# Optimization experiments

Measured on AMD Instinct MI355X. Metric: run time of the kernel, lower is better.

The kernel has to match this reference:

```python
import jax, jax.numpy as jnp
import numpy as np

N = 100000      # nodes
E = 3200000     # edges (avg degree 32)
IN_C = 256      # input feature dim
HID = 128       # hidden channels (= per-head dim, heads = 1)
L = 3           # num_layers_prop == num_layers_mlp
EPS = 1e-5


def _elu(x):
    return jnp.where(x > 0, x, jnp.expm1(x))


def _bn_eval(x, gamma, beta, mean, var):
    return (x - mean) * jax.lax.rsqrt(var + EPS) * gamma + beta


def _ln(x, gamma, beta):
    mu = jnp.mean(x, axis=-1, keepdims=True)
    var = jnp.var(x, axis=-1, keepdims=True)
    return (x - mu) * jax.lax.rsqrt(var + EPS) * gamma + beta


def setup_inputs() -> dict:
    key = jax.random.key(0)
    ks = jax.random.split(key, 12)
    s_in = np.float32(1.0 / np.sqrt(IN_C))
    s_h = np.float32(1.0 / np.sqrt(HID))
    return {
        "x": jax.random.normal(ks[0], (N, IN_C), jnp.float32),
        "edge_index": jax.random.randint(ks[1], (2, E), 0, N, jnp.int32),
        "mlp_W0": jax.random.normal(ks[2], (IN_C, HID), jnp.float32) * s_in,
        "mlp_b0": jnp.zeros((HID,), jnp.float32),
        "mlp_W": jax.random.normal(ks[3], (L - 1, HID, HID), jnp.float32) * s_h,
        "mlp_b": jnp.zeros((L - 1, HID), jnp.float32),
        "bn_gamma": jnp.ones((L, HID), jnp.float32),
        "bn_beta": jnp.zeros((L, HID), jnp.float32),
        "bn_mean": jnp.zeros((L, HID), jnp.float32),
        "bn_var": jnp.ones((L, HID), jnp.float32),
        "Wq": jax.random.normal(ks[4], (L, HID, HID), jnp.float32) * s_h,
        "bq": jnp.zeros((L, HID), jnp.float32),
        "Wk": jax.random.normal(ks[5], (L, HID, HID), jnp.float32) * s_h,
        "bk": jnp.zeros((L, HID), jnp.float32),
        "Wv": jax.random.normal(ks[6], (L, HID, HID), jnp.float32) * s_h,
        "bv": jnp.zeros((L, HID), jnp.float32),
        "Wg": jax.random.normal(ks[7], (L, HID, HID), jnp.float32) * s_h,
        "bg": jnp.zeros((L, HID), jnp.float32),
        "Wr": jax.random.normal(ks[8], (L, HID, HID), jnp.float32) * s_h,
        "br": jnp.zeros((L, HID), jnp.float32),
        "ln_gamma": jnp.ones((L, HID), jnp.float32),
        "ln_beta": jnp.zeros((L, HID), jnp.float32),
    }


def reference(x, edge_index, mlp_W0, mlp_b0, mlp_W, mlp_b, bn_gamma, bn_beta,
              bn_mean, bn_var, Wq, bq, Wk, bk, Wv, bv, Wg, bg, Wr, br,
              ln_gamma, ln_beta):
    n = x.shape[0]
    # --- mlp_in: Linear -> BN(eval) -> ELU, x3 (dropout p=0 skipped) ---
    h = _elu(_bn_eval(x @ mlp_W0 + mlp_b0, bn_gamma[0], bn_beta[0], bn_mean[0], bn_var[0]))
    for i in range(1, L):
        h = _elu(_bn_eval(h @ mlp_W[i - 1] + mlp_b[i - 1],
                          bn_gamma[i], bn_beta[i], bn_mean[i], bn_var[i]))

    # --- GCN edge normalization (shared across layers) ---
    row, col = edge_index[0], edge_index[1]
    deg = jax.ops.segment_sum(jnp.ones((E,), x.dtype), col, num_segments=n)
    val = jnp.sqrt(1.0 / deg[col]) * jnp.sqrt(1.0 / deg[row])
    val = jnp.nan_to_num(val, nan=0.0, posinf=0.0, neginf=0.0)

    # --- stacked TransConv layers (num_heads = 1) ---
    for i in range(L):
        prev = h
        q = h @ Wq[i] + bq[i]              # [N, M]
        k = h @ Wk[i] + bk[i]              # [N, M]
        v = h @ Wv[i] + bv[i]              # [N, D]
        qn = q / jnp.linalg.norm(q, axis=-1, keepdims=True)
        kn = k / jnp.linalg.norm(k, axis=-1, keepdims=True)
        kvs = kn.T @ v                     # [M, D]
        num = qn @ kvs + jnp.sum(v, axis=0)            # [N, D]
        denom = qn @ jnp.sum(kn, axis=0) + jnp.asarray(n, x.dtype)  # [N]
        attn_out = num / denom[:, None]    # heads=1 -> mean over heads is identity
        # sparse GCN: out[col] += val * gnn_in[row]
        g = h @ Wg[i] + bg[i]
        agg = jax.ops.segment_sum(val[:, None] * g[row], col, num_segments=n)
        out = attn_out + agg + (h @ Wr[i] + br[i])
        out = out + prev                   # outer residual in Transformer.forward
        h = _elu(_ln(out, ln_gamma[i], ln_beta[i]))
    return h
```

## Files before the change

### kernel.cpp

```cpp
#include <hip/hip_runtime.h>
#include <cstdint>
#include <cstddef>

#define HID 128
#define INC 256
#define NLAYER 3
#define SLOTS 96
#define P2G 16

static constexpr float EPS = 1e-5f;

typedef __attribute__((ext_vector_type(8))) short s16x8;
typedef __attribute__((ext_vector_type(4))) unsigned short us16x4;
typedef __attribute__((ext_vector_type(4))) float f32x4;
typedef __attribute__((ext_vector_type(2))) float f32x2;

__device__ __forceinline__ float eluf(float x) { return x > 0.f ? x : expm1f(x); }

__device__ __forceinline__ unsigned short f2bf(float x)
{
    unsigned u = __float_as_uint(x);
    u += 0x7FFFu + ((u >> 16) & 1u);
    return (unsigned short)(u >> 16);
}

__device__ __forceinline__ float bf2f(unsigned short u)
{
    return __uint_as_float(((unsigned)u) << 16);
}

__device__ __forceinline__ unsigned char f2fp8(float x)
{
    return (unsigned char)(__builtin_amdgcn_cvt_pk_fp8_f32(x, x, 0, false) & 0xFF);
}

__device__ __forceinline__ bool csr_side(int hostGrid, const int* __restrict__ ei,
                                         int* cnt, int* crow, int Etot, int e0, int e1)
{
    if ((int)blockIdx.x < hostGrid) return false;
    int e = e0 + (int)(blockIdx.x - hostGrid) * 256 + (int)threadIdx.x;
    if (e < e1) {
        int r = ei[e], c = ei[Etot + e];
        int p = atomicAdd(&cnt[c], 1);
        if (p < SLOTS) crow[(size_t)c * SLOTS + p] = r;
    }
    return true;
}

template<int K, bool IN32>
__global__ __launch_bounds__(256) void gemm_mlp(
    const float* __restrict__ Af, const unsigned short* __restrict__ A16,
    const unsigned short* __restrict__ Wth,
    const float* __restrict__ bias,
    const float* __restrict__ bng, const float* __restrict__ bnb,
    const float* __restrict__ bnm, const float* __restrict__ bnv,
    unsigned short* __restrict__ C16, int n,
    const int* __restrict__ ei, int* cntp, int* crowp, int Etot, int e0, int e1,
    int hostGrid)
{
    if (csr_side(hostGrid, ei, cntp, crowp, Etot, e0, e1)) return;

    __shared__ unsigned short Ah[64 * 64], Wh[128 * 64];
    const int t = threadIdx.x;
    const int l = t & 63;
    const int w = t >> 6;
    const int l15 = l & 15;
    const int row0 = blockIdx.x * 64;

    char* cAh = (char*)Ah;
    char* cWh = (char*)Wh;

    f32x4 acc[8] = {};

    for (int kc = 0; kc < K; kc += 64) {
        if (IN32) {
            #pragma unroll
            for (int i = 0; i < 4; ++i) {
                int f = t + 256 * i;
                int r = f >> 4, c4 = f & 15;
                int gr = row0 + r; if (gr > n - 1) gr = n - 1;
                float4 a4 = *(const float4*)&Af[(size_t)gr * K + kc + c4 * 4];
                int byte = r * 128 + (((c4 >> 1) * 16) ^ ((r & 7) << 4)) + (c4 & 1) * 8;
                *(us16x4*)(cAh + byte) =
                    (us16x4){f2bf(a4.x), f2bf(a4.y), f2bf(a4.z), f2bf(a4.w)};
            }
        } else {
            #pragma unroll
            for (int i = 0; i < 2; ++i) {
                int f = t + 256 * i;
                int r = f >> 3, c8 = f & 7;
                int gr = row0 + r; if (gr > n - 1) gr = n - 1;
                int byte = r * 128 + ((c8 * 16) ^ ((r & 7) << 4));
                *(s16x8*)(cAh + byte) = *(const s16x8*)&A16[(size_t)gr * K + kc + c8 * 8];
            }
        }
        #pragma unroll
        for (int i = 0; i < 4; ++i) {
            int f = t + 256 * i;
            int nr = f >> 3, c8 = f & 7;
            size_t gsrc = (size_t)nr * K + kc + c8 * 8;
            int byte = nr * 128 + ((c8 * 16) ^ ((nr & 7) << 4));
            *(s16x8*)(cWh + byte) = *(const s16x8*)&Wth[gsrc];
        }
        __syncthreads();
        #pragma unroll
        for (int ks = 0; ks < 2; ++ks) {
            int jA = ks * 4 + (l >> 4);
            int ar = w * 16 + l15;
            int aoff = ar * 128 + ((jA * 16) ^ ((ar & 7) << 4));
            s16x8 fah = *(s16x8*)(cAh + aoff);
            #pragma unroll
            for (int nt = 0; nt < 8; ++nt) {
                int nr = nt * 16 + l15;
                int boff = nr * 128 + ((jA * 16) ^ ((nr & 7) << 4));
                acc[nt] = __builtin_amdgcn_mfma_f32_16x16x32_bf16(fah, *(s16x8*)(cWh + boff), acc[nt], 0, 0, 0);
            }
        }
        __syncthreads();
    }

    const int rbase = row0 + w * 16 + ((l >> 4) << 2);
    #pragma unroll
    for (int nt = 0; nt < 8; ++nt) {
        int col = nt * 16 + l15;
        float bb = bias[col];
        float gm = bng[col], bt = bnb[col], mn = bnm[col], vr = bnv[col];
        #pragma unroll
        for (int r = 0; r < 4; ++r) {
            int row = rbase + r;
            if (row < n) {
                float o = acc[nt][r] + bb;
                o = eluf((o - mn) * rsqrtf(vr + EPS) * gm + bt);
                C16[(size_t)row * HID + col] = f2bf(o);
            }
        }
    }
}

struct QKVGRArgs {
    const unsigned short* wh[5];
    const float* bias[5];
};

__global__ __launch_bounds__(256) void fused_qkvgr(
    const unsigned short* __restrict__ A16, QKVGRArgs ar,
    unsigned short* __restrict__ qb16,
    unsigned char* __restrict__ gb8, float* __restrict__ accout,
    unsigned short* __restrict__ partial, int n,
    const int* __restrict__ ei, int* cntp, int* crowp, int Etot, int e0, int e1,
    int hostGrid)
{
    if (csr_side(hostGrid, ei, cntp, crowp, Etot, e0, e1)) return;

    __shared__ char smem[65536];
    char* cA  = smem;
    char* cW  = smem + 16384;
    char* cVT = smem + 49152;

    const int t = threadIdx.x;
    const int l = t & 63;
    const int w = t >> 6;
    const int l15 = l & 15;
    const int row0 = blockIdx.x * 64;

    #pragma unroll
    for (int i = 0; i < 4; ++i) {
        int f = t + 256 * i;
        int r = f >> 4, c8 = f & 15;
        int gr = row0 + r; if (gr > n - 1) gr = n - 1;
        int byte = r * 256 + ((c8 * 16) ^ ((r & 7) << 4));
        *(s16x8*)(cA + byte) = *(const s16x8*)&A16[(size_t)gr * HID + c8 * 8];
    }
    __syncthreads();

    s16x8 fah[4];
    {
        const int arow = w * 16 + l15;
        #pragma unroll
        for (int ks = 0; ks < 4; ++ks) {
            int aoff = arow * 256 + (((ks * 64) + (l >> 4) * 16) ^ ((arow & 7) << 4));
            fah[ks] = *(s16x8*)(cA + aoff);
        }
    }
    __syncthreads();

    const int rbase = row0 + w * 16 + ((l >> 4) << 2);
    const int rtb   = w * 16 + ((l >> 4) << 2);

    for (int m = 0; m < 5; ++m) {
        {
            const unsigned short* wh = ar.wh[m];
            #pragma unroll
            for (int i = 0; i < 8; ++i) {
                int f = t + 256 * i;
                int nr = f >> 4, c8 = f & 15;
                int byte = nr * 256 + ((c8 * 16) ^ ((nr & 7) << 4));
                *(s16x8*)(cW + byte) = *(const s16x8*)&wh[(size_t)nr * HID + c8 * 8];
            }
        }
        __syncthreads();

        f32x4 acc[8] = {};
        #pragma unroll
        for (int ks = 0; ks < 4; ++ks) {
            #pragma unroll
            for (int nt = 0; nt < 8; ++nt) {
                int nr = nt * 16 + l15;
                int boff = nr * 256 + (((ks * 64) + (l >> 4) * 16) ^ ((nr & 7) << 4));
                acc[nt] = __builtin_amdgcn_mfma_f32_16x16x32_bf16(fah[ks], *(s16x8*)(cW + boff), acc[nt], 0, 0, 0);
            }
        }

        float bb[8];
        #pragma unroll
        for (int nt = 0; nt < 8; ++nt) bb[nt] = ar.bias[m][nt * 16 + l15];

        if (m <= 1) {
            #pragma unroll
            for (int r = 0; r < 4; ++r) {
                float ss = 0.f;
                #pragma unroll
                for (int nt = 0; nt < 8; ++nt) {
                    float o = acc[nt][r] + bb[nt];
                    ss += o * o;
                }
                ss += __shfl_xor(ss, 1); ss += __shfl_xor(ss, 2);
                ss += __shfl_xor(ss, 4); ss += __shfl_xor(ss, 8);
                float rn = rsqrtf(ss);
                int row = rbase + r;
                if (m == 0) {
                    if (row < n) {
                        #pragma unroll
                        for (int nt = 0; nt < 8; ++nt)
                            qb16[(size_t)row * HID + nt * 16 + l15] = f2bf((acc[nt][r] + bb[nt]) * rn);
                    }
                } else {
                    int rt = rtb + r;
                    #pragma unroll
                    for (int nt = 0; nt < 8; ++nt) {
                        int kd = nt * 16 + l15;
                        unsigned short v16 = (row < n) ? f2bf((acc[nt][r] + bb[nt]) * rn) : (unsigned short)0;
                        int byte = kd * 128 + ((2 * rt) ^ ((kd & 7) << 4));
                        *(unsigned short*)(cA + byte) = v16;
                    }
                }
            }
        } else if (m == 2) {
            #pragma unroll
            for (int r = 0; r < 4; ++r) {
                int row = rbase + r;
                int rt = rtb + r;
                #pragma unroll
                for (int nt = 0; nt < 8; ++nt) {
                    int vd = nt * 16 + l15;
                    unsigned short v16 = (row < n) ? f2bf(acc[nt][r] + bb[nt]) : (unsigned short)0;
                    int byte = vd * 128 + ((2 * rt) ^ ((vd & 7) << 4));
                    *(unsigned short*)(cVT + byte) = v16;
                }
            }
        } else if (m == 3) {
            #pragma unroll
            for (int r = 0; r < 4; ++r) {
                int row = rbase + r;
                if (row < n) {
                    #pragma unroll
                    for (int nt = 0; nt < 8; ++nt)
                        gb8[(size_t)row * HID + nt * 16 + l15] = f2fp8(acc[nt][r] + bb[nt]);
                }
            }
        } else {
            #pragma unroll
            for (int r = 0; r < 4; ++r) {
                int row = rbase + r;
                if (row < n) {
                    #pragma unroll
                    for (int nt = 0; nt < 8; ++nt) {
                        int col = nt * 16 + l15;
                        accout[(size_t)row * HID + col] =
                            acc[nt][r] + bb[nt] + bf2f(A16[(size_t)row * HID + col]);
                    }
                }
            }
        }
        __syncthreads();
    }

    f32x4 kacc[2][8] = {};
    #pragma unroll
    for (int ks = 0; ks < 2; ++ks) {
        #pragma unroll
        for (int mt = 0; mt < 2; ++mt) {
            int kd = w * 32 + mt * 16 + l15;
            int aoff = kd * 128 + ((ks * 64 + (l >> 4) * 16) ^ ((kd & 7) << 4));
            s16x8 fa = *(s16x8*)(cA + aoff);
            #pragma unroll
            for (int nt = 0; nt < 8; ++nt) {
                int vd = nt * 16 + l15;
                int boff = vd * 128 + ((ks * 64 + (l >> 4) * 16) ^ ((vd & 7) << 4));
                kacc[mt][nt] = __builtin_amdgcn_mfma_f32_16x16x32_bf16(fa, *(s16x8*)(cVT + boff), kacc[mt][nt], 0, 0, 0);
            }
        }
    }
    unsigned short* pb = partial + (size_t)blockIdx.x * 16640;
    #pragma unroll
    for (int mt = 0; mt < 2; ++mt) {
        #pragma unroll
        for (int nt = 0; nt < 8; ++nt) {
            #pragma unroll
            for (int r = 0; r < 4; ++r) {
                int kd = w * 32 + mt * 16 + ((l >> 4) << 2) + r;
                pb[kd * 128 + nt * 16 + l15] = f2bf(kacc[mt][nt][r]);
            }
        }
    }
    {
        float s = 0.f;
        if (t < 128) {
            #pragma unroll 8
            for (int r = 0; r < 64; ++r) {
                int byte = t * 128 + ((2 * r) ^ ((t & 7) << 4));
                s += bf2f(*(unsigned short*)(cA + byte));
            }
            pb[16384 + t] = f2bf(s);
        } else {
            int vd = t - 128;
            #pragma unroll 8
            for (int r = 0; r < 64; ++r) {
                int byte = vd * 128 + ((2 * r) ^ ((vd & 7) << 4));
                s += bf2f(*(unsigned short*)(cVT + byte));
            }
            pb[16512 + vd] = f2bf(s);
        }
    }
}

__global__ __launch_bounds__(256) void gemm_num_combine(
    const unsigned short* __restrict__ A16,
    const unsigned short* __restrict__ Bth,
    const float* __restrict__ sumv, const float* __restrict__ snk,
    float nf, float* __restrict__ accio, int n,
    const int* __restrict__ ei, int* cntp, int* crowp, int Etot, int e0, int e1,
    int hostGrid)
{
    if (csr_side(hostGrid, ei, cntp, crowp, Etot, e0, e1)) return;

    __shared__ char smem[16384 + 32768];
    char* cA = smem;
    char* cW = smem + 16384;

    const int t = threadIdx.x;
    const int l = t & 63;
    const int w = t >> 6;
    const int l15 = l & 15;
    const int row0 = blockIdx.x * 64;

    #pragma unroll
    for (int i = 0; i < 4; ++i) {
        int f = t + 256 * i;
        int r = f >> 4, c8 = f & 15;
        int gr = row0 + r; if (gr > n - 1) gr = n - 1;
        int byte = r * 256 + ((c8 * 16) ^ ((r & 7) << 4));
        *(s16x8*)(cA + byte) = *(const s16x8*)&A16[(size_t)gr * HID + c8 * 8];
    }
    #pragma unroll
    for (int i = 0; i < 8; ++i) {
        int f = t + 256 * i;
        int nr = f >> 4, c8 = f & 15;
        int byte = nr * 256 + ((c8 * 16) ^ ((nr & 7) << 4));
        *(s16x8*)(cW + byte) = *(const s16x8*)&Bth[(size_t)nr * HID + c8 * 8];
    }
    __syncthreads();

    f32x4 acc[8] = {};
    const int arow = w * 16 + l15;
    #pragma unroll
    for (int ks = 0; ks < 4; ++ks) {
        int aoff = arow * 256 + (((ks * 64) + (l >> 4) * 16) ^ ((arow & 7) << 4));
        s16x8 fa = *(s16x8*)(cA + aoff);
        #pragma unroll
        for (int nt = 0; nt < 8; ++nt) {
            int nr = nt * 16 + l15;
            int boff = nr * 256 + (((ks * 64) + (l >> 4) * 16) ^ ((nr & 7) << 4));
            acc[nt] = __builtin_amdgcn_mfma_f32_16x16x32_bf16(fa, *(s16x8*)(cW + boff), acc[nt], 0, 0, 0);
        }
    }

    const int rbase = row0 + w * 16 + ((l >> 4) << 2);
    const int rtb   = w * 16 + ((l >> 4) << 2);
    float bb[8], skn[8];
    #pragma unroll
    for (int nt = 0; nt < 8; ++nt) {
        bb[nt]  = sumv[nt * 16 + l15];
        skn[nt] = snk[nt * 16 + l15];
    }
    #pragma unroll
    for (int r = 0; r < 4; ++r) {
        int row = rbase + r;
        int rt = rtb + r;
        float p = 0.f;
        #pragma unroll
        for (int nt = 0; nt < 8; ++nt) {
            int byte = rt * 256 + ((2 * (nt * 16 + l15)) ^ ((rt & 7) << 4));
            p += bf2f(*(unsigned short*)(cA + byte)) * skn[nt];
        }
        p += __shfl_xor(p, 1); p += __shfl_xor(p, 2);
        p += __shfl_xor(p, 4); p += __shfl_xor(p, 8);
        float dinv = 1.f / (p + nf);
        if (row < n) {
            #pragma unroll
            for (int nt = 0; nt < 8; ++nt) {
                size_t idx = (size_t)row * HID + nt * 16 + l15;
                accio[idx] += (acc[nt][r] + bb[nt]) * dinv;
            }
        }
    }
}

struct WConvArgs {
    const float* src[18];
    unsigned short* dh[18];
    int K[18];
};

__global__ void conv_weights(WConvArgs a)
{
    int m = blockIdx.x;
    const float* s = a.src[m];
    unsigned short* dh = a.dh[m];
    int K = a.K[m];
    int tot = 128 * K;
    int slice = (tot + gridDim.y - 1) / gridDim.y;
    int i0 = blockIdx.y * slice;
    int i1 = min(tot, i0 + slice);
    for (int idx = i0 + threadIdx.x; idx < i1; idx += 256) {
        int nn = idx / K, k = idx - nn * K;
        dh[idx] = f2bf(s[(size_t)k * 128 + nn]);
    }
}

__global__ __launch_bounds__(256) void reduce_kvs_p2a(
    const unsigned short* __restrict__ partial, int nb,
    float* __restrict__ partial2)
{
    const int oq = blockIdx.x * 256 + threadIdx.x;
    if (oq >= 4160) return;
    const int g   = blockIdx.y;
    const int per = (nb + P2G - 1) / P2G;
    const int b0  = g * per;
    const int b1  = min(nb, b0 + per);

    float s0 = 0.f, s1 = 0.f, s2 = 0.f, s3 = 0.f;
    int b = b0;
    for (; b + 3 < b1; b += 4) {
        us16x4 u0 = *(const us16x4*)&partial[(size_t)(b + 0) * 16640 + oq * 4];
        us16x4 u1 = *(const us16x4*)&partial[(size_t)(b + 1) * 16640 + oq * 4];
        us16x4 u2 = *(const us16x4*)&partial[(size_t)(b + 2) * 16640 + oq * 4];
        us16x4 u3 = *(const us16x4*)&partial[(size_t)(b + 3) * 16640 + oq * 4];
        s0 += bf2f(u0[0]) + bf2f(u1[0]) + bf2f(u2[0]) + bf2f(u3[0]);
        s1 += bf2f(u0[1]) + bf2f(u1[1]) + bf2f(u2[1]) + bf2f(u3[1]);
        s2 += bf2f(u0[2]) + bf2f(u1[2]) + bf2f(u2[2]) + bf2f(u3[2]);
        s3 += bf2f(u0[3]) + bf2f(u1[3]) + bf2f(u2[3]) + bf2f(u3[3]);
    }
    for (; b < b1; ++b) {
        us16x4 u0 = *(const us16x4*)&partial[(size_t)b * 16640 + oq * 4];
        s0 += bf2f(u0[0]); s1 += bf2f(u0[1]); s2 += bf2f(u0[2]); s3 += bf2f(u0[3]);
    }
    *(f32x4*)&partial2[(size_t)g * 16640 + oq * 4] = (f32x4){s0, s1, s2, s3};
}

__global__ __launch_bounds__(256) void reduce_kvs_p2b(
    const float* __restrict__ partial2,
    unsigned short* __restrict__ kvth, float* __restrict__ sums)
{
    int o = blockIdx.x * 256 + threadIdx.x;
    if (o >= 16640) return;
    float tot = 0.f;
    #pragma unroll
    for (int g = 0; g < P2G; ++g)
        tot += partial2[(size_t)g * 16640 + o];
    if (o < 16384) {
        int k = o >> 7, nn = o & 127;
        kvth[nn * 128 + k] = f2bf(tot);
    } else {
        sums[o - 16384] = tot;
    }
}

__global__ void rdeg_k(const int* __restrict__ cur, float* __restrict__ rdeg, int n)
{
    int i = blockIdx.x * 256 + threadIdx.x;
    if (i < n) {
        int c = cur[i];
        rdeg[i] = (c > 0) ? rsqrtf((float)c) : 0.f;
    }
}

__global__ __launch_bounds__(256) void gather_ln_elu4(
    const int* __restrict__ cnt, const int* __restrict__ crow,
    const float* __restrict__ rdeg,
    const unsigned char* __restrict__ g, const float* __restrict__ accin,
    const float* __restrict__ gam, const float* __restrict__ bet,
    float* __restrict__ outf, unsigned short* __restrict__ out16, int n)
{
    int node = (int)((blockIdx.x * 256 + threadIdx.x) >> 4);
    int li   = threadIdx.x & 15;
    if (node >= n) return;

    int cn = cnt[node]; if (cn > SLOTS) cn = SLOTS;
    const int* cr = &crow[(size_t)node * SLOTS];
    float rd = rdeg[node];
    const unsigned b8 = (unsigned)li * 8u;
    float4 a0 = *(const float4*)&accin[(size_t)node * HID + li * 8];
    float4 a1 = *(const float4*)&accin[(size_t)node * HID + li * 8 + 4];

    auto acc8 = [&](uint2 U_, float W_) {
        f32x2 pa = __builtin_amdgcn_cvt_pk_f32_fp8((int)U_.x, false);
        f32x2 pb = __builtin_amdgcn_cvt_pk_f32_fp8((int)U_.x, true);
        f32x2 pc = __builtin_amdgcn_cvt_pk_f32_fp8((int)U_.y, false);
        f32x2 pd = __builtin_amdgcn_cvt_pk_f32_fp8((int)U_.y, true);
        a0.x += W_ * pa[0]; a0.y += W_ * pa[1];
        a0.z += W_ * pb[0]; a0.w += W_ * pb[1];
        a1.x += W_ * pc[0]; a1.y += W_ * pc[1];
        a1.z += W_ * pd[0]; a1.w += W_ * pd[1];
    };

    int i = 0;
    for (; i + 3 < cn; i += 4) {
        int   r0 = cr[i],     r1 = cr[i + 1];
        int   r2 = cr[i + 2], r3 = cr[i + 3];
        float w0 = rd * rdeg[r0], w1 = rd * rdeg[r1];
        float w2 = rd * rdeg[r2], w3 = rd * rdeg[r3];
        uint2 u0 = *(const uint2*)&g[(unsigned)r0 * 128u + b8];
        uint2 u1 = *(const uint2*)&g[(unsigned)r1 * 128u + b8];
        uint2 u2 = *(const uint2*)&g[(unsigned)r2 * 128u + b8];
        uint2 u3 = *(const uint2*)&g[(unsigned)r3 * 128u + b8];
        acc8(u0, w0); acc8(u1, w1); acc8(u2, w2); acc8(u3, w3);
    }
    for (; i < cn; ++i) {
        int r0 = cr[i];
        float w0 = rd * rdeg[r0];
        uint2 u0 = *(const uint2*)&g[(unsigned)r0 * 128u + b8];
        acc8(u0, w0);
    }

    float sm = a0.x + a0.y + a0.z + a0.w + a1.x + a1.y + a1.z + a1.w;
    float ss = a0.x * a0.x + a0.y * a0.y + a0.z * a0.z + a0.w * a0.w
             + a1.x * a1.x + a1.y * a1.y + a1.z * a1.z + a1.w * a1.w;
    #pragma unroll
    for (int o = 8; o; o >>= 1) { sm += __shfl_xor(sm, o); ss += __shfl_xor(ss, o); }
    float mu  = sm * (1.f / 128.f);
    float var = ss * (1.f / 128.f) - mu * mu;
    float rs  = rsqrtf(var + EPS);
    float4 gm0 = *(const float4*)&gam[li * 8];
    float4 gm1 = *(const float4*)&gam[li * 8 + 4];
    float4 bt0 = *(const float4*)&bet[li * 8];
    float4 bt1 = *(const float4*)&bet[li * 8 + 4];
    float y0 = eluf((a0.x - mu) * rs * gm0.x + bt0.x);
    float y1 = eluf((a0.y - mu) * rs * gm0.y + bt0.y);
    float y2 = eluf((a0.z - mu) * rs * gm0.z + bt0.z);
    float y3 = eluf((a0.w - mu) * rs * gm0.w + bt0.w);
    float y4 = eluf((a1.x - mu) * rs * gm1.x + bt1.x);
    float y5 = eluf((a1.y - mu) * rs * gm1.y + bt1.y);
    float y6 = eluf((a1.z - mu) * rs * gm1.z + bt1.z);
    float y7 = eluf((a1.w - mu) * rs * gm1.w + bt1.w);
    if (out16) {
        us16x4 o0 = (us16x4){f2bf(y0), f2bf(y1), f2bf(y2), f2bf(y3)};
        us16x4 o1 = (us16x4){f2bf(y4), f2bf(y5), f2bf(y6), f2bf(y7)};
        *(us16x4*)&out16[(size_t)node * HID + li * 8]     = o0;
        *(us16x4*)&out16[(size_t)node * HID + li * 8 + 4] = o1;
    } else {
        *(float4*)&outf[(size_t)node * HID + li * 8]     = make_float4(y0, y1, y2, y3);
        *(float4*)&outf[(size_t)node * HID + li * 8 + 4] = make_float4(y4, y5, y6, y7);
    }
}

extern "C" void kernel_launch(void* const* d_in, const int* in_sizes, int n_in,
                              void* d_out, int out_size, void* d_ws, size_t ws_size,
                              hipStream_t stream)
{
    const float* x      = (const float*)d_in[0];
    const int*   ei     = (const int*)  d_in[1];
    const float* mlp_W0 = (const float*)d_in[2];
    const float* mlp_b0 = (const float*)d_in[3];
    const float* mlp_W  = (const float*)d_in[4];
    const float* mlp_b  = (const float*)d_in[5];
    const float* bn_g   = (const float*)d_in[6];
    const float* bn_b   = (const float*)d_in[7];
    const float* bn_m   = (const float*)d_in[8];
    const float* bn_v   = (const float*)d_in[9];
    const float* Wq = (const float*)d_in[10]; const float* bq = (const float*)d_in[11];
    const float* Wk = (const float*)d_in[12]; const float* bk = (const float*)d_in[13];
    const float* Wv = (const float*)d_in[14]; const float* bv = (const float*)d_in[15];
    const float* Wg = (const float*)d_in[16]; const float* bg = (const float*)d_in[17];
    const float* Wr = (const float*)d_in[18]; const float* br = (const float*)d_in[19];
    const float* ln_g = (const float*)d_in[20];
    const float* ln_b = (const float*)d_in[21];

    const int N = in_sizes[0] / INC;
    const int E = in_sizes[1] / 2;
    const size_t P = (size_t)N * HID;
    const int gemmGrid = (N + 63) / 64;

    unsigned short* partial = (unsigned short*)d_ws;
    size_t partUS = (size_t)gemmGrid * 16640;
    if (partUS < P) partUS = P;
    unsigned short* h16  = partial + partUS;
    unsigned short* qb16 = h16 + P;
    unsigned char*  gb8  = (unsigned char*)(qb16 + P);
    float* kvs  = (float*)(gb8 + P);
    float* partial2 = kvs + 256;
    int*   crow = (int*)(partial2 + (size_t)P2G * 16640);
    int*   cnt  = crow + (size_t)N * SLOTS;
    float* rdeg = (float*)(cnt + N);
    unsigned short* wt = (unsigned short*)(rdeg + N);

    unsigned short* mlpA = partial;
    unsigned short* mlpB = qb16;

    unsigned short* WTh[18];
    int Ks[18];
    size_t woff = 0;
    for (int m = 0; m < 18; ++m) {
        int K = (m == 0) ? INC : HID;
        Ks[m] = K;
        WTh[m] = wt + woff;           woff += (size_t)128 * K;
    }
    unsigned short* kvth = wt + woff; woff += 16384;
    float* acc = (float*)d_out;

    const int gw4Grid  = (N + 15) / 16;
    const int nodeGrid = (N + 255) / 256;

    int eb[6];
    for (int i = 0; i <= 5; ++i) eb[i] = (int)(((long long)E * i) / 5);
    auto cb = [&](int i) { return (eb[i + 1] - eb[i] + 255) / 256; };

    WConvArgs wa;
    const float* srcs[18];
    srcs[0] = mlp_W0; srcs[1] = mlp_W; srcs[2] = mlp_W + (size_t)HID * HID;
    for (int l = 0; l < NLAYER; ++l) {
        const size_t wo = (size_t)l * HID * HID;
        srcs[3 + l * 5 + 0] = Wq + wo;
        srcs[3 + l * 5 + 1] = Wk + wo;
        srcs[3 + l * 5 + 2] = Wv + wo;
        srcs[3 + l * 5 + 3] = Wg + wo;
        srcs[3 + l * 5 + 4] = Wr + wo;
    }
    for (int m = 0; m < 18; ++m) {
        wa.src[m] = srcs[m]; wa.dh[m] = WTh[m]; wa.K[m] = Ks[m];
    }
    conv_weights<<<dim3(18, 8), 256, 0, stream>>>(wa);

    hipMemsetAsync(cnt, 0, (size_t)N * sizeof(int), stream);

    gemm_mlp<INC, true><<<gemmGrid + cb(0), 256, 0, stream>>>(x, nullptr, WTh[0], mlp_b0,
        bn_g, bn_b, bn_m, bn_v, mlpA, N, ei, cnt, crow, E, eb[0], eb[1], gemmGrid);
    gemm_mlp<HID, false><<<gemmGrid + cb(1), 256, 0, stream>>>(nullptr, mlpA, WTh[1], mlp_b,
        bn_g + HID, bn_b + HID, bn_m + HID, bn_v + HID, mlpB, N,
        ei, cnt, crow, E, eb[1], eb[2], gemmGrid);
    gemm_mlp<HID, false><<<gemmGrid + cb(2), 256, 0, stream>>>(nullptr, mlpB, WTh[2], mlp_b + HID,
        bn_g + 2 * HID, bn_b + 2 * HID, bn_m + 2 * HID, bn_v + 2 * HID, h16, N,
        ei, cnt, crow, E, eb[2], eb[3], gemmGrid);

    for (int l = 0; l < NLAYER; ++l) {
        const int bo = l * HID;
        const bool l0 = (l == 0);

        QKVGRArgs qa;
        for (int m = 0; m < 5; ++m) qa.wh[m] = WTh[3 + l * 5 + m];
        qa.bias[0] = bq + bo; qa.bias[1] = bk + bo; qa.bias[2] = bv + bo;
        qa.bias[3] = bg + bo; qa.bias[4] = br + bo;

        fused_qkvgr<<<gemmGrid + (l0 ? cb(3) : 0), 256, 0, stream>>>(h16, qa,
            qb16, gb8, acc, partial, N,
            ei, cnt, crow, E, l0 ? eb[3] : 0, l0 ? eb[4] : 0, gemmGrid);

        reduce_kvs_p2a<<<dim3(17, P2G), 256, 0, stream>>>(partial, gemmGrid, partial2);
        reduce_kvs_p2b<<<65, 256, 0, stream>>>(partial2, kvth, kvs);

        gemm_num_combine<<<gemmGrid + (l0 ? cb(4) : 0), 256, 0, stream>>>(qb16, kvth,
            kvs + 128, kvs, (float)N, acc, N,
            ei, cnt, crow, E, l0 ? eb[4] : 0, l0 ? eb[5] : 0, gemmGrid);

        if (l0) rdeg_k<<<nodeGrid, 256, 0, stream>>>(cnt, rdeg, N);

        bool last = (l == NLAYER - 1);
        gather_ln_elu4<<<gw4Grid, 256, 0, stream>>>(cnt, crow, rdeg,
            gb8, acc, ln_g + bo, ln_b + bo,
            last ? acc : nullptr, last ? nullptr : h16, N);
    }
}
```

Measured before the change: 764.4 us.

## Prefetch next weight matrix into registers and fuse column sums into epilogue

The fused QKVGR kernel now issues the global loads for the next projection's weight matrix into registers before the current MFMA loop runs. After the current stage it writes them to shared memory, so global latency overlaps with compute. It also computes the per-block sums of normalized k and of v during the existing epilogue, using warp shuffles and a small shared array, in place of a final serial pass over shared memory. This costs extra registers, which may lower occupancy, and adds one more barrier per stage. The sums are now taken from fp32 values rather than bf16-rounded ones.

```diff
diff --git a/kernel.cpp b/kernel.cpp
--- a/kernel.cpp
+++ b/kernel.cpp
@@ -153,6 +153,8 @@
     if (csr_side(hostGrid, ei, cntp, crowp, Etot, e0, e1)) return;
 
     __shared__ char smem[65536];
+    __shared__ float sks[4][128];
+    __shared__ float svs[4][128];
     char* cA  = smem;
     char* cW  = smem + 16384;
     char* cVT = smem + 49152;
@@ -182,23 +184,32 @@
             fah[ks] = *(s16x8*)(cA + aoff);
         }
     }
+    {
+        const unsigned short* wh = ar.wh[0];
+        #pragma unroll
+        for (int i = 0; i < 8; ++i) {
+            int f = t + 256 * i;
+            int nr = f >> 4, c8 = f & 15;
+            int byte = nr * 256 + ((c8 * 16) ^ ((nr & 7) << 4));
+            *(s16x8*)(cW + byte) = *(const s16x8*)&wh[(size_t)nr * HID + c8 * 8];
+        }
+    }
     __syncthreads();
 
     const int rbase = row0 + w * 16 + ((l >> 4) << 2);
     const int rtb   = w * 16 + ((l >> 4) << 2);
 
     for (int m = 0; m < 5; ++m) {
-        {
-            const unsigned short* wh = ar.wh[m];
+        s16x8 wreg[8];
+        if (m < 4) {
+            const unsigned short* wh = ar.wh[m + 1];
             #pragma unroll
             for (int i = 0; i < 8; ++i) {
                 int f = t + 256 * i;
                 int nr = f >> 4, c8 = f & 15;
-                int byte = nr * 256 + ((c8 * 16) ^ ((nr & 7) << 4));
-                *(s16x8*)(cW + byte) = *(const s16x8*)&wh[(size_t)nr * HID + c8 * 8];
-            }
-        }
-        __syncthreads();
+                wreg[i] = *(const s16x8*)&wh[(size_t)nr * HID + c8 * 8];
+            }
+        }
 
         f32x4 acc[8] = {};
         #pragma unroll
@@ -216,6 +227,7 @@
         for (int nt = 0; nt < 8; ++nt) bb[nt] = ar.bias[m][nt * 16 + l15];
 
         if (m <= 1) {
+            float sk8[8] = {};
             #pragma unroll
             for (int r = 0; r < 4; ++r) {
                 float ss = 0.f;
@@ -236,27 +248,50 @@
                     }
                 } else {
                     int rt = rtb + r;
+                    bool ok = (row < n);
                     #pragma unroll
                     for (int nt = 0; nt < 8; ++nt) {
                         int kd = nt * 16 + l15;
-                        unsigned short v16 = (row < n) ? f2bf((acc[nt][r] + bb[nt]) * rn) : (unsigned short)0;
+                        float on = (acc[nt][r] + bb[nt]) * rn;
+                        unsigned short v16 = ok ? f2bf(on) : (unsigned short)0;
                         int byte = kd * 128 + ((2 * rt) ^ ((kd & 7) << 4));
                         *(unsigned short*)(cA + byte) = v16;
+                        sk8[nt] += ok ? on : 0.f;
                     }
                 }
             }
+            if (m == 1) {
+                #pragma unroll
+                for (int nt = 0; nt < 8; ++nt) {
+                    float s = sk8[nt];
+                    s += __shfl_xor(s, 16);
+                    s += __shfl_xor(s, 32);
+                    if (l < 16) sks[w][nt * 16 + l15] = s;
+                }
+            }
         } else if (m == 2) {
+            float sv8[8] = {};
             #pragma unroll
             for (int r = 0; r < 4; ++r) {
                 int row = rbase + r;
                 int rt = rtb + r;
+                bool ok = (row < n);
                 #pragma unroll
                 for (int nt = 0; nt < 8; ++nt) {
                     int vd = nt * 16 + l15;
-                    unsigned short v16 = (row < n) ? f2bf(acc[nt][r] + bb[nt]) : (unsigned short)0;
+                    float on = acc[nt][r] + bb[nt];
+                    unsigned short v16 = ok ? f2bf(on) : (unsigned short)0;
                     int byte = vd * 128 + ((2 * rt) ^ ((vd & 7) << 4));
                     *(unsigned short*)(cVT + byte) = v16;
+                    sv8[nt] += ok ? on : 0.f;
                 }
+            }
+            #pragma unroll
+            for (int nt = 0; nt < 8; ++nt) {
+                float s = sv8[nt];
+                s += __shfl_xor(s, 16);
+                s += __shfl_xor(s, 32);
+                if (l < 16) svs[w][nt * 16 + l15] = s;
             }
         } else if (m == 3) {
             #pragma unroll
@@ -283,6 +318,16 @@
             }
         }
         __syncthreads();
+        if (m < 4) {
+            #pragma unroll
+            for (int i = 0; i < 8; ++i) {
+                int f = t + 256 * i;
+                int nr = f >> 4, c8 = f & 15;
+                int byte = nr * 256 + ((c8 * 16) ^ ((nr & 7) << 4));
+                *(s16x8*)(cW + byte) = wreg[i];
+            }
+        }
+        __syncthreads();
     }
 
     f32x4 kacc[2][8] = {};
@@ -313,24 +358,11 @@
             }
         }
     }
-    {
-        float s = 0.f;
-        if (t < 128) {
-            #pragma unroll 8
-            for (int r = 0; r < 64; ++r) {
-                int byte = t * 128 + ((2 * r) ^ ((t & 7) << 4));
-                s += bf2f(*(unsigned short*)(cA + byte));
-            }
-            pb[16384 + t] = f2bf(s);
-        } else {
-            int vd = t - 128;
-            #pragma unroll 8
-            for (int r = 0; r < 64; ++r) {
-                int byte = vd * 128 + ((2 * r) ^ ((vd & 7) << 4));
-                s += bf2f(*(unsigned short*)(cVT + byte));
-            }
-            pb[16512 + vd] = f2bf(s);
-        }
+    if (t < 128) {
+        pb[16384 + t] = f2bf(sks[0][t] + sks[1][t] + sks[2][t] + sks[3][t]);
+    } else {
+        int vd = t - 128;
+        pb[16512 + vd] = f2bf(svs[0][vd] + svs[1][vd] + svs[2][vd] + svs[3][vd]);
     }
 }
 
```

After: 861.7 us. 1.13x slower.
